# Kernel optimization log

Hardware: AMD Instinct MI355X
Metric: run time of the kernel (lower is better)

## Reference

```python
import jax, jax.numpy as jnp
import numpy as np

H, KV, D = 16, 4, 128
EPS = 1e-6

def setup_inputs() -> dict:
    key = jax.random.key(0)
    ks = jax.random.split(key, 7)
    B, S, HS = 2, 2048, 2048
    return {
        "hidden_states": jax.random.normal(ks[0], (B, S, HS), jnp.float32),
        "cos": jax.random.uniform(ks[1], (S, D), jnp.float32),
        "sin": jax.random.uniform(ks[2], (S, D), jnp.float32),
        "Wq": jax.random.normal(ks[3], (H * D, HS), jnp.float32) * 0.02,
        "Wk": jax.random.normal(ks[4], (KV * D, HS), jnp.float32) * 0.02,
        "Wv": jax.random.normal(ks[5], (KV * D, HS), jnp.float32) * 0.02,
        "Wo": jax.random.normal(ks[6], (HS, H * D), jnp.float32) * 0.02,
        "norm_q_w": jnp.ones((D,), jnp.float32),
        "norm_k_w": jnp.ones((D,), jnp.float32),
    }

def _rmsnorm(x, w):
    # RMSNorm over head_dim
    return x * jax.lax.rsqrt(jnp.mean(x * x, axis=-1, keepdims=True) + EPS) * w

def _rope(x, cos, sin):
    # x: [B, S, heads, D]; cos/sin: [S, D]; rotate-half (use_real_unbind_dim=-2)
    c = cos[None, :, None, :]
    s = sin[None, :, None, :]
    x1, x2 = jnp.split(x, 2, axis=-1)
    x_rot = jnp.concatenate([-x2, x1], axis=-1)
    return x * c + x_rot * s

def reference(hidden_states, cos, sin, Wq, Wk, Wv, Wo, norm_q_w, norm_k_w):
    B, S, _ = hidden_states.shape
    q = (hidden_states @ Wq.T).reshape(B, S, H, D)
    k = (hidden_states @ Wk.T).reshape(B, S, KV, D)
    v = (hidden_states @ Wv.T).reshape(B, S, KV, D)
    q = _rmsnorm(q, norm_q_w)
    k = _rmsnorm(k, norm_k_w)
    q = _rope(q, cos, sin)
    k = _rope(k, cos, sin)
    # GQA: repeat_interleave K/V heads to match Q heads
    g = H // KV
    k = jnp.repeat(k, g, axis=2)  # [B, S, H, D]
    v = jnp.repeat(v, g, axis=2)
    scores = jnp.einsum('bqhd,bkhd->bhqk', q, k) * (D ** -0.5)
    attn = jax.nn.softmax(scores, axis=-1)
    out = jnp.einsum('bhqk,bkhd->bqhd', attn, v)  # [B, S, H, D]
    out = out.reshape(B, S, H * D)
    return out @ Wo.T
```

## Files before the change

kernel.cpp:

```cpp
#include <hip/hip_runtime.h>


typedef __attribute__((ext_vector_type(8))) short bf16x8;
typedef __attribute__((ext_vector_type(4))) float f32x4;
typedef __attribute__((ext_vector_type(16))) float f32x16;

__device__ __forceinline__ unsigned short f2bf(float x) {
  union { float f; unsigned u; } v; v.f = x;
  unsigned r = v.u + 0x7fffu + ((v.u >> 16) & 1u);
  return (unsigned short)(r >> 16);
}

__device__ __forceinline__ float bf2f(unsigned short h) {
  union { unsigned u; float f; } v; v.u = (unsigned)h << 16;
  return v.f;
}

__device__ __forceinline__ unsigned cvt_pk_bf16(float lo, float hi) {
  unsigned r;
  asm("v_cvt_pk_bf16_f32 %0, %1, %2" : "=v"(r) : "v"(lo), "v"(hi));
  return r;
}

__device__ __forceinline__ void gload_lds16(const void* g, void* l) {
  __builtin_amdgcn_global_load_lds(
      (const __attribute__((address_space(1))) void*)g,
      (__attribute__((address_space(3))) void*)l, 16, 0, 0);
}

__global__ __launch_bounds__(256) void cvt4(const float4* __restrict__ in,
                                            ushort4* __restrict__ out, int n4) {
  int i = blockIdx.x * 256 + threadIdx.x;
  if (i < n4) {
    float4 v = in[i];
    out[i] = make_ushort4(f2bf(v.x), f2bf(v.y), f2bf(v.z), f2bf(v.w));
  }
}

template <int NF, bool OUT_BF16>
__global__ __launch_bounds__(512, 2) void gemm_bt_8ph(
    const unsigned short* __restrict__ A, const unsigned short* __restrict__ Bm,
    void* __restrict__ Cout, int M, int N, int K) {
  __shared__ char lsA[2][32768];
  __shared__ char lsB[2][NF * 8192];
  const int tid = threadIdx.x;
  const int wave = tid >> 6, lane = tid & 63;
  const int lrow = lane & 15, kg = lane >> 4;
  const int wm = wave >> 2, wn = wave & 3;
  const int BN = NF * 64;
  const int nbn = N / BN;
  const int bid = (blockIdx.x & 7) * (gridDim.x >> 3) + (blockIdx.x >> 3);
  const int m0 = (bid / nbn) << 8;
  const int n0 = (bid % nbn) * BN;
  const int NT = K >> 6;

  const int srow = tid >> 2;
  const int scol = (((tid & 3) ^ (srow & 3)) << 3);
  const size_t a0 = (size_t)(m0 + srow) * K + scol;
  const size_t a1 = (size_t)(m0 + 128 + srow) * K + scol;
  const size_t b0 = (size_t)(n0 + srow) * K + scol;
  const size_t b1 = (size_t)(n0 + 128 + srow) * K + scol;

  f32x4 acc[8][NF];
#pragma unroll
  for (int i = 0; i < 8; ++i)
#pragma unroll
    for (int j = 0; j < NF; ++j)
#pragma unroll
      for (int t = 0; t < 4; ++t) acc[i][j][t] = 0.f;

  const int xk = ((kg ^ (lrow & 3)) << 4);
  const int abase = (wm * 128 + lrow) * 64 + xk;
  const int bbase = (wn * NF * 16 + lrow) * 64 + xk;

  auto stage_plane = [&](int T, int ks) {
    if (T >= NT) return;
    const int buf = T & 1;
    const size_t kof = (size_t)T * 64 + ks * 32;
    char* da = lsA[buf] + ks * 16384 + wave * 1024;
    gload_lds16(A + a0 + kof, da);
    gload_lds16(A + a1 + kof, da + 8192);
    char* db = lsB[buf] + ks * (NF * 4096) + wave * 1024;
    gload_lds16(Bm + b0 + kof, db);
    if (NF >= 3) {
      if (tid < 256) gload_lds16(Bm + b1 + kof, db + 8192);
    }
  };

  auto phase = [&](int T, int ks, int sT, int sKs) {
    const int buf = T & 1;
    const char* pa = lsA[buf] + ks * 16384;
    const char* pb = lsB[buf] + ks * (NF * 4096);
    bf16x8 af[8], bfr[NF];
#pragma unroll
    for (int mf = 0; mf < 8; ++mf)
      af[mf] = *(const bf16x8*)(pa + abase + mf * 1024);
#pragma unroll
    for (int nf = 0; nf < NF; ++nf)
      bfr[nf] = *(const bf16x8*)(pb + bbase + nf * 1024);
    stage_plane(sT, sKs);
    asm volatile("s_waitcnt vmcnt(6)" ::: "memory");
    __builtin_amdgcn_s_barrier();
    asm volatile("s_waitcnt lgkmcnt(0)" ::: "memory");
    __builtin_amdgcn_sched_barrier(0);
    __builtin_amdgcn_s_setprio(1);
#pragma unroll
    for (int mf = 0; mf < 8; ++mf)
#pragma unroll
      for (int nf = 0; nf < NF; ++nf)
        acc[mf][nf] =
            __builtin_amdgcn_mfma_f32_16x16x32_bf16(af[mf], bfr[nf], acc[mf][nf], 0, 0, 0);
    __builtin_amdgcn_s_setprio(0);
    __builtin_amdgcn_s_barrier();
  };

  stage_plane(0, 0);
  stage_plane(0, 1);
  stage_plane(1, 0);
  asm volatile("s_waitcnt vmcnt(6)" ::: "memory");
  __builtin_amdgcn_s_barrier();

  for (int kt = 0; kt < NT; ++kt) {
    phase(kt, 0, kt + 1, 1);
    phase(kt, 1, kt + 2, 0);
  }

#pragma unroll
  for (int mf = 0; mf < 8; ++mf) {
#pragma unroll
    for (int nf = 0; nf < NF; ++nf) {
      int row = m0 + wm * 128 + mf * 16 + kg * 4;
      int col = n0 + wn * NF * 16 + nf * 16 + lrow;
      if (OUT_BF16) {
        unsigned short* C = (unsigned short*)Cout;
#pragma unroll
        for (int t = 0; t < 4; ++t)
          C[(size_t)(row + t) * N + col] = f2bf(acc[mf][nf][t]);
      } else {
        float* C = (float*)Cout;
#pragma unroll
        for (int t = 0; t < 4; ++t)
          C[(size_t)(row + t) * N + col] = acc[mf][nf][t];
      }
    }
  }
}

__global__ __launch_bounds__(256) void rms_rope(
    const unsigned short* __restrict__ QKV, const float* __restrict__ cosT,
    const float* __restrict__ sinT, const float* __restrict__ wq,
    const float* __restrict__ wk, unsigned short* __restrict__ Q,
    unsigned short* __restrict__ Kg, unsigned short* __restrict__ Vg) {
  int task = blockIdx.x * 4 + (threadIdx.x >> 6);
  int lane = threadIdx.x & 63;
  int row = task / 24;
  int slot = task - row * 24;
  int b = row >> 11, s = row & 2047;
  const unsigned short* x = QKV + (size_t)row * 3072 + slot * 128;
  float x1 = bf2f(x[lane]), x2 = bf2f(x[lane + 64]);
  if (slot < 20) {
    float ss = x1 * x1 + x2 * x2;
#pragma unroll
    for (int msk = 1; msk < 64; msk <<= 1) ss += __shfl_xor(ss, msk);
    float inv = rsqrtf(ss * (1.0f / 128.0f) + 1e-6f);
    const float* w = (slot < 16) ? wq : wk;
    x1 *= inv * w[lane];
    x2 *= inv * w[lane + 64];
    float c1 = cosT[s * 128 + lane], c2 = cosT[s * 128 + lane + 64];
    float sn1 = sinT[s * 128 + lane], sn2 = sinT[s * 128 + lane + 64];
    float o1 = x1 * c1 - x2 * sn1;
    float o2 = x2 * c2 + x1 * sn2;
    if (slot < 16) {
      const float qs = 0.08838834764831845f * 1.4426950408889634f;
      o1 *= qs; o2 *= qs;
    }
    x1 = o1; x2 = o2;
  }
  if (slot < 16) {
    unsigned short* dst = Q + (((size_t)b * 16 + slot) * 2048 + s) * 128;
    dst[lane] = f2bf(x1);
    dst[lane + 64] = f2bf(x2);
  } else {
    int kv = (slot - 16) & 3;
    size_t tb = ((size_t)((b * 4 + kv) * 32) + (s >> 6)) * 16384;
    int key = s & 63;
    if (slot < 20) {
      char* base = (char*)Kg + tb;
      int xr = (key & 7) << 4;
      *(unsigned short*)(base + key * 256 + ((lane * 2) ^ xr)) = f2bf(x1);
      *(unsigned short*)(base + key * 256 + (((lane + 64) * 2) ^ xr)) = f2bf(x2);
    } else {
      char* base = (char*)Vg + tb;
      int p = key >> 4;
      int vhi = (key >> 2) & 1;
      int e = (key & 3) | (((key >> 3) & 1) << 2);
      int off = p * 4096 + vhi * 512 + e * 2;
      int d1 = lane, d2 = lane + 64;
      *(unsigned short*)(base + off + (d1 >> 5) * 1024 + (d1 & 31) * 16) = f2bf(x1);
      *(unsigned short*)(base + off + (d2 >> 5) * 1024 + (d2 & 31) * 16) = f2bf(x2);
    }
  }
}

__global__ __launch_bounds__(256, 2) void attn64(
    const unsigned short* __restrict__ Q, const unsigned short* __restrict__ Kg,
    const unsigned short* __restrict__ Vg, unsigned short* __restrict__ O) {
  __shared__ unsigned short Kl[2][8192];
  __shared__ unsigned short Vl[2][8192];
  const int tid = threadIdx.x;
  const int wave = tid >> 6, lane = tid & 63;
  const int l31 = lane & 31, hi = lane >> 5;
  int bid = blockIdx.x;
  bid = (bid & 7) * 64 + (bid >> 3);
  const int bh = bid >> 4, qt = bid & 15;
  const int b = bh >> 4, h = bh & 15, kh = h >> 2;
  const char* Kt = (const char*)Kg + (size_t)(b * 4 + kh) * 524288;
  const char* Vt = (const char*)Vg + (size_t)(b * 4 + kh) * 524288;
  const unsigned short* Qb =
      Q + ((size_t)(b * 16 + h) * 2048 + qt * 128 + wave * 32) * 128;
  bf16x8 qf[8];
#pragma unroll
  for (int s = 0; s < 8; ++s)
    qf[s] = *(const bf16x8*)(Qb + l31 * 128 + s * 16 + hi * 8);
  f32x16 acc[4];
#pragma unroll
  for (int c = 0; c < 4; ++c)
#pragma unroll
    for (int r = 0; r < 16; ++r) acc[c][r] = 0.f;
  float lsum = 0.f;
  const int xrk = (l31 & 7) << 4;

  auto stage = [&](int t) {
    const char* kt = Kt + (size_t)t * 16384;
    const char* vt = Vt + (size_t)t * 16384;
    char* kd = (char*)Kl[t & 1];
    char* vd = (char*)Vl[t & 1];
#pragma unroll
    for (int c = 0; c < 4; ++c) {
      gload_lds16(kt + c * 4096 + tid * 16, kd + c * 4096 + wave * 1024);
      gload_lds16(vt + c * 4096 + tid * 16, vd + c * 4096 + wave * 1024);
    }
  };

  auto qk = [&](int t, f32x16& s0, f32x16& s1) {
    const char* Kb = (const char*)Kl[t & 1];
#pragma unroll
    for (int r = 0; r < 16; ++r) { s0[r] = 0.f; s1[r] = 0.f; }
#pragma unroll
    for (int s = 0; s < 8; ++s) {
      int xo = (s * 32 + hi * 16) ^ xrk;
      bf16x8 k0 = *(const bf16x8*)(Kb + l31 * 256 + xo);
      bf16x8 k1 = *(const bf16x8*)(Kb + (32 + l31) * 256 + xo);
      s0 = __builtin_amdgcn_mfma_f32_32x32x16_bf16(k0, qf[s], s0, 0, 0, 0);
      s1 = __builtin_amdgcn_mfma_f32_32x32x16_bf16(k1, qf[s], s1, 0, 0, 0);
    }
  };

  auto body = [&](int t, f32x16& c0, f32x16& c1, f32x16& n0_, f32x16& n1_) {
    float p0[16], p1[16];
#pragma unroll
    for (int r = 0; r < 16; ++r) {
      p0[r] = exp2f(c0[r]);
      p1[r] = exp2f(c1[r]);
    }
    float u8[8];
#pragma unroll
    for (int r = 0; r < 8; ++r) u8[r] = (p0[r] + p0[r + 8]) + (p1[r] + p1[r + 8]);
#pragma unroll
    for (int r = 0; r < 4; ++r) u8[r] += u8[r + 4];
    lsum += (u8[0] + u8[1]) + (u8[2] + u8[3]);
    union { bf16x8 v[4]; unsigned w[16]; } pa;
#pragma unroll
    for (int r = 0; r < 4; ++r) {
      pa.w[r]      = cvt_pk_bf16(p0[2 * r], p0[2 * r + 1]);
      pa.w[4 + r]  = cvt_pk_bf16(p0[8 + 2 * r], p0[9 + 2 * r]);
      pa.w[8 + r]  = cvt_pk_bf16(p1[2 * r], p1[2 * r + 1]);
      pa.w[12 + r] = cvt_pk_bf16(p1[8 + 2 * r], p1[9 + 2 * r]);
    }
    __syncthreads();
    __builtin_amdgcn_s_setprio(1);
    if (t + 1 < 32) qk(t + 1, n0_, n1_);
    const char* Vb = (const char*)Vl[t & 1];
#pragma unroll
    for (int p = 0; p < 4; ++p)
#pragma unroll
      for (int c = 0; c < 4; ++c) {
        bf16x8 vf = *(const bf16x8*)(Vb + p * 4096 + c * 1024 + hi * 512 + l31 * 16);
        acc[c] = __builtin_amdgcn_mfma_f32_32x32x16_bf16(pa.v[p], vf, acc[c], 0, 0, 0);
      }
    __builtin_amdgcn_s_setprio(0);
    __syncthreads();
    if (t + 2 < 32) stage(t + 2);
  };

  stage(0);
  __syncthreads();
  f32x16 s0A, s1A, s0B, s1B;
  qk(0, s0A, s1A);
  stage(1);

  for (int t = 0; t < 32; t += 2) {
    body(t, s0A, s1A, s0B, s1B);
    body(t + 1, s0B, s1B, s0A, s1A);
  }

  lsum += __shfl_xor(lsum, 32);
  float inv = 1.0f / lsum;
#pragma unroll
  for (int r = 0; r < 16; ++r) {
    int q = (r & 3) + 8 * (r >> 2) + 4 * hi;
    float invq = __shfl(inv, q);
    int srow = qt * 128 + wave * 32 + q;
    unsigned short* dst = O + (((size_t)b * 2048 + srow) * 16 + h) * 128;
#pragma unroll
    for (int c = 0; c < 4; ++c)
      dst[c * 32 + l31] = f2bf(acc[c][r] * invq);
  }
}

extern "C" void kernel_launch(void* const* d_in, const int* in_sizes, int n_in,
                              void* d_out, int out_size, void* d_ws, size_t ws_size,
                              hipStream_t stream) {
  const float* hs   = (const float*)d_in[0];
  const float* cosT = (const float*)d_in[1];
  const float* sinT = (const float*)d_in[2];
  const float* Wq   = (const float*)d_in[3];
  const float* Wk   = (const float*)d_in[4];
  const float* Wv   = (const float*)d_in[5];
  const float* Wo   = (const float*)d_in[6];
  const float* nqw  = (const float*)d_in[7];
  const float* nkw  = (const float*)d_in[8];
  float* out = (float*)d_out;

  char* ws = (char*)d_ws;
  unsigned short* X    = (unsigned short*)ws;
  unsigned short* Wqkv = X + 8388608;
  unsigned short* WoB  = Wqkv + 6291456;
  unsigned short* QKVb = WoB + 4194304;
  unsigned short* Qb   = QKVb + 12582912;
  unsigned short* Kg   = Qb + 8388608;
  unsigned short* Vg   = Kg + 2097152;
  unsigned short* Ob   = QKVb;

  cvt4<<<8192, 256, 0, stream>>>((const float4*)hs, (ushort4*)X, 2097152);
  cvt4<<<4096, 256, 0, stream>>>((const float4*)Wq, (ushort4*)Wqkv, 1048576);
  cvt4<<<1024, 256, 0, stream>>>((const float4*)Wk, (ushort4*)(Wqkv + 4194304), 262144);
  cvt4<<<1024, 256, 0, stream>>>((const float4*)Wv, (ushort4*)(Wqkv + 5242880), 262144);
  cvt4<<<4096, 256, 0, stream>>>((const float4*)Wo, (ushort4*)WoB, 1048576);

  gemm_bt_8ph<3, true><<<256, 512, 0, stream>>>(X, Wqkv, QKVb, 4096, 3072, 2048);

  rms_rope<<<24576, 256, 0, stream>>>(QKVb, cosT, sinT, nqw, nkw, Qb, Kg, Vg);

  attn64<<<512, 256, 0, stream>>>(Qb, Kg, Vg, Ob);

  gemm_bt_8ph<2, false><<<256, 512, 0, stream>>>(Ob, WoB, out, 4096, 2048, 2048);
}
```

Measured before the change: 225.7 us.

## Merge conversion launches, re-layout K tiles, and reorder attention QK scheduling

```diff
diff --git a/kernel.cpp b/kernel.cpp
--- a/kernel.cpp
+++ b/kernel.cpp
@@ -28,13 +28,23 @@
       (__attribute__((address_space(3))) void*)l, 16, 0, 0);
 }
 
-__global__ __launch_bounds__(256) void cvt4(const float4* __restrict__ in,
-                                            ushort4* __restrict__ out, int n4) {
+__global__ __launch_bounds__(256) void cvt_all(
+    const float4* __restrict__ hs, const float4* __restrict__ wq,
+    const float4* __restrict__ wk, const float4* __restrict__ wv,
+    const float4* __restrict__ wo, ushort4* __restrict__ X,
+    ushort4* __restrict__ Wqkv, ushort4* __restrict__ WoB) {
   int i = blockIdx.x * 256 + threadIdx.x;
-  if (i < n4) {
-    float4 v = in[i];
-    out[i] = make_ushort4(f2bf(v.x), f2bf(v.y), f2bf(v.z), f2bf(v.w));
-  }
+  const float4* src;
+  ushort4* dst;
+  int off;
+  if (i < 2097152)      { src = hs; dst = X;               off = 0; }
+  else if (i < 3145728) { src = wq; dst = Wqkv;            off = 2097152; }
+  else if (i < 3407872) { src = wk; dst = Wqkv + 1048576;  off = 3145728; }
+  else if (i < 3670016) { src = wv; dst = Wqkv + 1310720;  off = 3407872; }
+  else                  { src = wo; dst = WoB;             off = 3670016; }
+  int j = i - off;
+  float4 v = src[j];
+  dst[j] = make_ushort4(f2bf(v.x), f2bf(v.y), f2bf(v.z), f2bf(v.w));
 }
 
 template <int NF, bool OUT_BF16>
@@ -186,9 +196,10 @@
     int key = s & 63;
     if (slot < 20) {
       char* base = (char*)Kg + tb;
-      int xr = (key & 7) << 4;
-      *(unsigned short*)(base + key * 256 + ((lane * 2) ^ xr)) = f2bf(x1);
-      *(unsigned short*)(base + key * 256 + (((lane + 64) * 2) ^ xr)) = f2bf(x2);
+      int kb = (key >> 5) * 512 + (key & 31) * 16;
+      int d1 = lane, d2 = lane + 64;
+      *(unsigned short*)(base + (d1 >> 4) * 2048 + ((d1 >> 3) & 1) * 1024 + kb + (d1 & 7) * 2) = f2bf(x1);
+      *(unsigned short*)(base + (d2 >> 4) * 2048 + ((d2 >> 3) & 1) * 1024 + kb + (d2 & 7) * 2) = f2bf(x2);
     } else {
       char* base = (char*)Vg + tb;
       int p = key >> 4;
@@ -228,7 +239,6 @@
 #pragma unroll
     for (int r = 0; r < 16; ++r) acc[c][r] = 0.f;
   float lsum = 0.f;
-  const int xrk = (l31 & 7) << 4;
 
   auto stage = [&](int t) {
     const char* kt = Kt + (size_t)t * 16384;
@@ -243,20 +253,21 @@
   };
 
   auto qk = [&](int t, f32x16& s0, f32x16& s1) {
-    const char* Kb = (const char*)Kl[t & 1];
+    const char* Kb = (const char*)Kl[t & 1] + hi * 1024 + l31 * 16;
 #pragma unroll
     for (int r = 0; r < 16; ++r) { s0[r] = 0.f; s1[r] = 0.f; }
+    __builtin_amdgcn_s_setprio(1);
 #pragma unroll
     for (int s = 0; s < 8; ++s) {
-      int xo = (s * 32 + hi * 16) ^ xrk;
-      bf16x8 k0 = *(const bf16x8*)(Kb + l31 * 256 + xo);
-      bf16x8 k1 = *(const bf16x8*)(Kb + (32 + l31) * 256 + xo);
+      bf16x8 k0 = *(const bf16x8*)(Kb + s * 2048);
+      bf16x8 k1 = *(const bf16x8*)(Kb + s * 2048 + 512);
       s0 = __builtin_amdgcn_mfma_f32_32x32x16_bf16(k0, qf[s], s0, 0, 0, 0);
       s1 = __builtin_amdgcn_mfma_f32_32x32x16_bf16(k1, qf[s], s1, 0, 0, 0);
     }
-  };
-
-  auto body = [&](int t, f32x16& c0, f32x16& c1, f32x16& n0_, f32x16& n1_) {
+    __builtin_amdgcn_s_setprio(0);
+  };
+
+  auto half = [&](int t, f32x16& c0, f32x16& c1, f32x16& n0_, f32x16& n1_) {
     float p0[16], p1[16];
 #pragma unroll
     for (int r = 0; r < 16; ++r) {
@@ -278,9 +289,8 @@
       pa.w[12 + r] = cvt_pk_bf16(p1[8 + 2 * r], p1[9 + 2 * r]);
     }
     __syncthreads();
+    const char* Vb = (const char*)Vl[t & 1];
     __builtin_amdgcn_s_setprio(1);
-    if (t + 1 < 32) qk(t + 1, n0_, n1_);
-    const char* Vb = (const char*)Vl[t & 1];
 #pragma unroll
     for (int p = 0; p < 4; ++p)
 #pragma unroll
@@ -291,17 +301,19 @@
     __builtin_amdgcn_s_setprio(0);
     __syncthreads();
     if (t + 2 < 32) stage(t + 2);
+    __builtin_amdgcn_sched_barrier(0);
+    if (t + 1 < 32) qk(t + 1, n0_, n1_);
   };
 
   stage(0);
   __syncthreads();
-  f32x16 s0A, s1A, s0B, s1B;
-  qk(0, s0A, s1A);
+  f32x16 sA0, sA1, sB0, sB1;
+  qk(0, sA0, sA1);
   stage(1);
 
   for (int t = 0; t < 32; t += 2) {
-    body(t, s0A, s1A, s0B, s1B);
-    body(t + 1, s0B, s1B, s0A, s1A);
+    half(t, sA0, sA1, sB0, sB1);
+    half(t + 1, sB0, sB1, sA0, sA1);
   }
 
   lsum += __shfl_xor(lsum, 32);
@@ -342,11 +354,10 @@
   unsigned short* Vg   = Kg + 2097152;
   unsigned short* Ob   = QKVb;
 
-  cvt4<<<8192, 256, 0, stream>>>((const float4*)hs, (ushort4*)X, 2097152);
-  cvt4<<<4096, 256, 0, stream>>>((const float4*)Wq, (ushort4*)Wqkv, 1048576);
-  cvt4<<<1024, 256, 0, stream>>>((const float4*)Wk, (ushort4*)(Wqkv + 4194304), 262144);
-  cvt4<<<1024, 256, 0, stream>>>((const float4*)Wv, (ushort4*)(Wqkv + 5242880), 262144);
-  cvt4<<<4096, 256, 0, stream>>>((const float4*)Wo, (ushort4*)WoB, 1048576);
+  cvt_all<<<18432, 256, 0, stream>>>((const float4*)hs, (const float4*)Wq,
+                                     (const float4*)Wk, (const float4*)Wv,
+                                     (const float4*)Wo, (ushort4*)X,
+                                     (ushort4*)Wqkv, (ushort4*)WoB);
 
   gemm_bt_8ph<3, true><<<256, 512, 0, stream>>>(X, Wqkv, QKVb, 4096, 3072, 2048);
 
```

After: 220.2 us. 2.4% less time.
